# Kernel tuning notes

Measured on AMD Instinct MI355X. Metric: run time of the kernel, lower is better.

## Reference

```python
import jax, jax.numpy as jnp
import numpy as np

N = 50000          # nodes
E = 1_600_000      # edges (avg degree 32)
F = 64             # num_features == hidden dim of every layer
R = 5              # num_rel (edge ratings)
B = 4              # num_base (basis decomposition)
L = 4              # number of RGCN layers (dim=[64,64,64,64])
K = 2048           # nodes with x[:,0]==1 (target user/item nodes)


def setup_inputs() -> dict:
    key = jax.random.key(0)
    ks = jax.random.split(key, 10)
    x = jax.random.normal(ks[0], (N, F), dtype=jnp.float32)
    target_idx = jnp.arange(K, dtype=jnp.int32)
    # mark exactly K target nodes: x[:,0] == 1 iff node index < K
    col0 = (jnp.arange(N) < K).astype(jnp.float32)
    x = x.at[:, 0].set(col0)
    edge_index = jax.random.randint(ks[1], (2, E), 0, N, dtype=jnp.int32)
    edge_type = jax.random.randint(ks[2], (E,), 0, R, dtype=jnp.int32)
    s = 1.0 / np.sqrt(F)
    bases = jax.random.normal(ks[3], (L, B, F, F), dtype=jnp.float32) * s
    comps = jax.random.normal(ks[4], (L, R, B), dtype=jnp.float32) * (1.0 / np.sqrt(B))
    roots = jax.random.normal(ks[5], (L, F, F), dtype=jnp.float32) * s
    biases = jnp.zeros((L, F), dtype=jnp.float32)
    w1 = jax.random.normal(ks[6], (2 * L * F, 128), dtype=jnp.float32) * (1.0 / np.sqrt(2 * L * F))
    b1 = jnp.zeros((128,), dtype=jnp.float32)
    w2 = jax.random.normal(ks[7], (128, 1), dtype=jnp.float32) * (1.0 / np.sqrt(128))
    b2 = jnp.zeros((1,), dtype=jnp.float32)
    return {"x": x, "edge_index": edge_index, "edge_type": edge_type,
            "target_idx": target_idx, "bases": bases, "comps": comps,
            "roots": roots, "biases": biases, "w1": w1, "b1": b1,
            "w2": w2, "b2": b2}


def _rgcn_layer(x, src, dst, etype, bases_l, comp_l, root_l, bias_l):
    # basis decomposition: W_r = sum_b comp[r,b] * bases[b]   -> [R, in, out]
    W = jnp.einsum('rb,bio->rio', comp_l, bases_l)
    # transform every node under every relation, then gather per edge
    H = jnp.einsum('ni,rio->rno', x, W)          # [R, N, out]
    m = H[etype, src]                            # [E, out] per-edge messages
    # per-(target node, relation) MEAN aggregation (PyG RGCNConv semantics)
    seg = dst * R + etype                        # [E]
    sums = jax.ops.segment_sum(m, seg, num_segments=N * R)
    cnts = jax.ops.segment_sum(jnp.ones((m.shape[0],), dtype=x.dtype), seg,
                               num_segments=N * R)
    mean = sums / jnp.maximum(cnts, 1.0)[:, None]
    agg = mean.reshape(N, R, -1).sum(axis=1)     # sum over relations
    return agg + x @ root_l + bias_l


def reference(x, edge_index, edge_type, target_idx, bases, comps, roots,
              biases, w1, b1, w2, b2):
    # inference mode: edge dropout / feature dropout are identity
    src, dst = edge_index[0], edge_index[1]
    h = x
    h_i = []
    for l in range(L):
        h = jnp.tanh(_rgcn_layer(h, src, dst, edge_type,
                                 bases[l], comps[l], roots[l], biases[l]))
        h_i.append(h)
    h_cat = jnp.concatenate(h_i, axis=1)         # [N, sum(dim)] = [N, 256]
    # u and i masks are identical in the source (x[:,0]==1); target_idx holds
    # exactly those node indices, so index gather == boolean mask selection.
    sel = h_cat[target_idx]                      # [K, 256]
    feat = jnp.concatenate([sel, sel], axis=1)   # [K, 512]
    hid = jax.nn.relu(feat @ w1 + b1)
    out = hid @ w2 + b2
    return out[:, 0]
```

## Files before the change

### kernel.cpp

```cpp
#include <hip/hip_runtime.h>
#include <hip/hip_bf16.h>

#define Nn 50000
#define Ee 1600000
#define Ff 64
#define Rr 5
#define Bb 4
#define Ll 4
#define Kk 2048
#define NBK 196
#define SEGB 1280
#define MsegP (NBK*SEGB)
#define NTC ((Nn+63)/64)
#define NCH ((Ee+8191)/8192)
#define WTSL (12*4*64*8)

typedef __attribute__((ext_vector_type(8))) short short8;
typedef __attribute__((ext_vector_type(4))) float v4f;

static __device__ __forceinline__ unsigned short f2b(float f){
  unsigned u = __float_as_uint(f);
  unsigned r = (u + 0x7fffu + ((u>>16)&1u)) >> 16;
  return (unsigned short)r;
}
static __device__ __forceinline__ unsigned packbf(float lo, float hi){
  return (unsigned)f2b(lo) | ((unsigned)f2b(hi) << 16);
}
static __device__ __forceinline__ float2 unpackbf(unsigned u){
  return make_float2(__uint_as_float(u << 16), __uint_as_float(u & 0xffff0000u));
}

#define XB_B 6250
#define IV_B (XB_B+196)
#define WE_B (IV_B+128)
#define WS_B (WE_B+48)
#define TF_B (WS_B+4)
#define MS_B (TF_B+1)
__global__ __launch_bounds__(256) void k_setupA(const float* __restrict__ x, unsigned* __restrict__ xb,
    int* __restrict__ inv, const float* __restrict__ w1, float* __restrict__ w1e,
    const float* __restrict__ bases, const float* __restrict__ comps, const float* __restrict__ roots,
    unsigned short* __restrict__ WTs, int* __restrict__ tflag, int* __restrict__ bcnt,
    unsigned* __restrict__ hA, unsigned* __restrict__ hB)
{
  int b = blockIdx.x, t = threadIdx.x;
  if (b < XB_B){
    int idx = b*256 + t;
    int n = idx >> 5, j = idx & 31;
    float2 v = *(const float2*)&x[(size_t)n*64 + 2*j];
    xb[idx] = packbf(v.x, v.y);
  } else if (b < IV_B){
    int i = (b-XB_B)*256 + t;
    if (i < Nn) inv[i] = -1;
  } else if (b < WE_B){
    int idx = (b-IV_B)*256 + t;
    int i = idx >> 7, j = idx & 127;
    w1e[idx] = w1[i*128 + j] + w1[(i+256)*128 + j];
  } else if (b < WS_B){
    int gid = (b-WE_B)*256 + t;
    int lane = gid & 63, nb = (gid>>6)&3, idx2 = gid>>8;
    int l = idx2/12, kk = idx2 - l*12;
    int o = nb*16 + (lane & 15);
    int kbase = kk*32 + (lane>>4)*8;
    const float* basesl = bases + (size_t)l*Bb*Ff*Ff;
    const float* compsl = comps + (size_t)l*Rr*Bb;
    const float* rootsl = roots + (size_t)l*Ff*Ff;
    unsigned short* wp = WTs + (size_t)gid*8;
    #pragma unroll
    for (int j=0;j<8;j++){
      int k = kbase + j;
      float s;
      if (k < 320){
        int c = k >> 6, i = k & 63;
        s = 0.f;
        #pragma unroll
        for (int bb2=0;bb2<Bb;bb2++)
          s += compsl[c*Bb+bb2] * basesl[(bb2*Ff + i)*Ff + o];
      } else {
        s = rootsl[(k-320)*Ff + o];
      }
      wp[j] = f2b(s);
    }
  } else if (b < TF_B){
    int i = (b-WS_B)*256 + t;
    if (i < NTC) tflag[i] = 0;
  } else {
    if (t < NBK+1) bcnt[t] = 0;
    if (t < 32){
      xb[(size_t)Nn*32 + t] = 0;
      hA[(size_t)Nn*32 + t] = 0;
      hB[(size_t)Nn*32 + t] = 0;
    }
  }
}

__global__ __launch_bounds__(256) void k_setupB(const int* __restrict__ tidx, int* __restrict__ inv,
                                                int* __restrict__ tflag){
  int k = blockIdx.x*256+threadIdx.x;
  if (k < Kk){
    int n = tidx[k];
    inv[n] = k;
    tflag[n >> 6] = 1;
  }
}

__global__ __launch_bounds__(256) void k_bcnt(const int* __restrict__ ei, int* __restrict__ bcnt){
  __shared__ int h[NBK];
  int t = threadIdx.x;
  for (int i=t;i<NBK;i+=256) h[i]=0;
  __syncthreads();
  int base = blockIdx.x*8192;
  for (int i=0;i<32;i++){
    int e = base + i*256 + t;
    if (e < Ee) atomicAdd(&h[ei[Ee+e]>>8], 1);
  }
  __syncthreads();
  for (int i=t;i<NBK;i+=256) if (h[i]) atomicAdd(&bcnt[i], h[i]);
}

__global__ __launch_bounds__(256) void k_bscan(const int* __restrict__ bcnt, int* __restrict__ bbase,
                                               int* __restrict__ bfill, int* __restrict__ rowptr){
  __shared__ int s[256];
  int t = threadIdx.x;
  int v = (t < NBK) ? bcnt[t] : 0;
  s[t] = v; __syncthreads();
  #pragma unroll
  for (int off=1; off<256; off<<=1){
    int x = (t>=off) ? s[t-off] : 0;
    __syncthreads();
    s[t] += x;
    __syncthreads();
  }
  if (t < NBK){ int ex = s[t]-v; bbase[t]=ex; bfill[t]=ex; }
  if (t == 0){ bbase[NBK] = Ee; rowptr[MsegP] = Ee; }
}

__global__ __launch_bounds__(256) void k_bin(const int* __restrict__ ei, const int* __restrict__ et,
                                             int* __restrict__ bfill, unsigned* __restrict__ ebin){
  __shared__ unsigned led[8192];
  __shared__ int h[NBK], gb[NBK];
  int t = threadIdx.x;
  for (int i=t;i<NBK;i+=256) h[i]=0;
  __syncthreads();
  int base = blockIdx.x*8192;
  for (int i=0;i<32;i++){
    int e = base + i*256 + t;
    if (e < Ee){
      int src = ei[e];
      int dst = ei[Ee+e];
      int r = et[e];
      led[i*256+t] = (unsigned)src | ((unsigned)(dst&255)<<16) | ((unsigned)r<<24);
      atomicAdd(&h[dst>>8], 1);
    }
  }
  __syncthreads();
  for (int i=t;i<NBK;i+=256) if (h[i]){ gb[i] = atomicAdd(&bfill[i], h[i]); h[i] = 0; }
  __syncthreads();
  for (int i=0;i<32;i++){
    int e = base + i*256 + t;
    if (e < Ee){
      int b = ei[Ee+e]>>8;
      int off = atomicAdd(&h[b], 1);
      ebin[gb[b]+off] = led[i*256+t];
    }
  }
}

__global__ __launch_bounds__(512) void k_sort(const unsigned* __restrict__ ebin, const int* __restrict__ bbase,
                                              unsigned short* __restrict__ srcs, int* __restrict__ rowptr){
  __shared__ int cntA[SEGB], excA[SEGB];
  int b = blockIdx.x, t = threadIdx.x;
  int base = bbase[b], cnt = bbase[b+1]-base;
  for (int i=t;i<SEGB;i+=512) cntA[i]=0;
  __syncthreads();
  for (int i=t;i<cnt;i+=512){
    unsigned u = ebin[base+i];
    int segl = (int)((u>>24)&7u)*256 + (int)((u>>16)&255u);
    atomicAdd(&cntA[segl], 1);
  }
  __syncthreads();
  for (int i=t;i<SEGB;i+=512) excA[i]=cntA[i];
  __syncthreads();
  for (int off=1; off<SEGB; off<<=1){
    int i0=t, i1=t+512, i2=t+1024;
    int v0 = (i0>=off)? excA[i0-off] : 0;
    int v1 = (i1>=off)? excA[i1-off] : 0;
    int v2 = (i2<SEGB && i2>=off)? excA[i2-off] : 0;
    __syncthreads();
    excA[i0]+=v0;
    excA[i1]+=v1;
    if (i2<SEGB) excA[i2]+=v2;
    __syncthreads();
  }
  for (int i=t;i<SEGB;i+=512){
    int ex = excA[i]-cntA[i];
    excA[i] = ex;
    rowptr[b*SEGB+i] = base + ex;
    cntA[i] = 0;
  }
  __syncthreads();
  for (int i=t;i<cnt;i+=512){
    unsigned u = ebin[base+i];
    int segl = (int)((u>>24)&7u)*256 + (int)((u>>16)&255u);
    int off = atomicAdd(&cntA[segl], 1);
    srcs[base + excA[segl] + off] = (unsigned short)(u & 0xffffu);
  }
}

static __device__ __forceinline__ void gpass(int mys, float* A, int p, int half5, int sub, int li,
                                             const unsigned* __restrict__ h2)
{
  int s0 = __shfl(mys, half5 + p +      sub, 64);
  int s1 = __shfl(mys, half5 + p +  4 + sub, 64);
  int s2 = __shfl(mys, half5 + p +  8 + sub, 64);
  int s3 = __shfl(mys, half5 + p + 12 + sub, 64);
  uint4 g0 = *(const uint4*)&h2[(size_t)s0*32 + li*4];
  uint4 g1 = *(const uint4*)&h2[(size_t)s1*32 + li*4];
  uint4 g2 = *(const uint4*)&h2[(size_t)s2*32 + li*4];
  uint4 g3 = *(const uint4*)&h2[(size_t)s3*32 + li*4];
  float2 f;
  f=unpackbf(g0.x); A[0]+=f.x; A[1]+=f.y;  f=unpackbf(g0.y); A[2]+=f.x; A[3]+=f.y;
  f=unpackbf(g0.z); A[4]+=f.x; A[5]+=f.y;  f=unpackbf(g0.w); A[6]+=f.x; A[7]+=f.y;
  f=unpackbf(g1.x); A[0]+=f.x; A[1]+=f.y;  f=unpackbf(g1.y); A[2]+=f.x; A[3]+=f.y;
  f=unpackbf(g1.z); A[4]+=f.x; A[5]+=f.y;  f=unpackbf(g1.w); A[6]+=f.x; A[7]+=f.y;
  f=unpackbf(g2.x); A[0]+=f.x; A[1]+=f.y;  f=unpackbf(g2.y); A[2]+=f.x; A[3]+=f.y;
  f=unpackbf(g2.z); A[4]+=f.x; A[5]+=f.y;  f=unpackbf(g2.w); A[6]+=f.x; A[7]+=f.y;
  f=unpackbf(g3.x); A[0]+=f.x; A[1]+=f.y;  f=unpackbf(g3.y); A[2]+=f.x; A[3]+=f.y;
  f=unpackbf(g3.z); A[4]+=f.x; A[5]+=f.y;  f=unpackbf(g3.w); A[6]+=f.x; A[7]+=f.y;
}

static __device__ __forceinline__ void tail_gather(float* A, int s, int e, int li,
    const unsigned short* __restrict__ srcs, const unsigned* __restrict__ h2)
{
  for (int i = s; i < e; i++){
    uint4 g = *(const uint4*)&h2[(size_t)srcs[i]*32 + li*4];
    float2 f;
    f=unpackbf(g.x); A[0]+=f.x; A[1]+=f.y;  f=unpackbf(g.y); A[2]+=f.x; A[3]+=f.y;
    f=unpackbf(g.z); A[4]+=f.x; A[5]+=f.y;  f=unpackbf(g.w); A[6]+=f.x; A[7]+=f.y;
  }
}

__global__ __launch_bounds__(256) void k_seg(const unsigned short* __restrict__ srcs,
    const int* __restrict__ rowptr, const unsigned* __restrict__ h2, unsigned* __restrict__ y2)
{
  int tid = threadIdx.x;
  int hw = tid >> 5;
  int l2 = tid & 31, li = l2 & 7, sub = l2 >> 3;
  int half5 = tid & 32;
  int wl = tid & 63;
  int sA = blockIdx.x*16 + hw*2;
  int b = sA / SEGB;
  int segl = sA - b*SEGB;
  int r = segl >> 8;
  int dstA = b*256 + (segl & 255);
  int2 pp = *(const int2*)&rowptr[sA];
  int p2 = rowptr[sA+2];
  int degA = pp.y - pp.x, degB = p2 - pp.y;
  unsigned ldA = srcs[pp.x + l2];
  unsigned ldB = srcs[pp.y + l2];
  int mysA = (l2 < degA) ? (int)ldA : Nn;
  int mysB = (l2 < degB) ? (int)ldB : Nn;
  float aA[8] = {0.f,0.f,0.f,0.f,0.f,0.f,0.f,0.f};
  float aB[8] = {0.f,0.f,0.f,0.f,0.f,0.f,0.f,0.f};

  gpass(mysA, aA, 0, half5, sub, li, h2);
  gpass(mysB, aB, 0, half5, sub, li, h2);
  if (degA > 16) gpass(mysA, aA, 16, half5, sub, li, h2);
  if (degB > 16) gpass(mysB, aB, 16, half5, sub, li, h2);

  if (sub == 0){
    if (degA > 32) tail_gather(aA, pp.x+32, pp.y, li, srcs, h2);
    if (degB > 32) tail_gather(aB, pp.y+32, p2,   li, srcs, h2);
  }
  #pragma unroll
  for (int k=0;k<8;k++){
    aA[k] += __shfl(aA[k], wl^8, 64);
    aB[k] += __shfl(aB[k], wl^8, 64);
  }
  #pragma unroll
  for (int k=0;k<8;k++){
    aA[k] += __shfl(aA[k], wl^16, 64);
    aB[k] += __shfl(aB[k], wl^16, 64);
  }
  if (sub == 0){
    if (dstA < Nn){
      float sc = (degA > 0) ? 1.0f/(float)degA : 0.f;
      uint4 o;
      o.x = packbf(aA[0]*sc, aA[1]*sc);
      o.y = packbf(aA[2]*sc, aA[3]*sc);
      o.z = packbf(aA[4]*sc, aA[5]*sc);
      o.w = packbf(aA[6]*sc, aA[7]*sc);
      *(uint4*)&y2[((size_t)r*Nn + dstA)*32 + li*4] = o;
    }
    if (dstA + 1 < Nn){
      float sc = (degB > 0) ? 1.0f/(float)degB : 0.f;
      uint4 o;
      o.x = packbf(aB[0]*sc, aB[1]*sc);
      o.y = packbf(aB[2]*sc, aB[3]*sc);
      o.z = packbf(aB[4]*sc, aB[5]*sc);
      o.w = packbf(aB[6]*sc, aB[7]*sc);
      *(uint4*)&y2[((size_t)r*Nn + dstA + 1)*32 + li*4] = o;
    }
  }
}

__global__ __launch_bounds__(256) void k_seg_t(const unsigned short* __restrict__ srcs,
    const int* __restrict__ rowptr, const unsigned* __restrict__ h2, unsigned* __restrict__ y2,
    const int* __restrict__ tidx)
{
  int idx = blockIdx.x*8 + (threadIdx.x >> 5);
  if (idx >= Rr*Kk) return;
  int r = idx >> 11;
  int k = idx & (Kk-1);
  int dst = tidx[k];
  int s2 = (dst>>8)*SEGB + r*256 + (dst&255);
  int tid = threadIdx.x;
  int l2 = tid & 31, li = l2 & 7, sub = l2 >> 3;
  int half5 = tid & 32;
  int wl = tid & 63;
  int s = rowptr[s2], e = rowptr[s2+1];
  int deg = e - s;
  unsigned ld = srcs[s + l2];
  int mys = (l2 < deg) ? (int)ld : Nn;
  float a[8] = {0.f,0.f,0.f,0.f,0.f,0.f,0.f,0.f};
  gpass(mys, a, 0, half5, sub, li, h2);
  if (deg > 16) gpass(mys, a, 16, half5, sub, li, h2);
  if (deg > 32 && sub == 0) tail_gather(a, s+32, e, li, srcs, h2);
  #pragma unroll
  for (int q=0;q<8;q++) a[q] += __shfl(a[q], wl^8, 64);
  #pragma unroll
  for (int q=0;q<8;q++) a[q] += __shfl(a[q], wl^16, 64);
  if (sub == 0){
    float sc = (deg > 0) ? 1.0f/(float)deg : 0.f;
    uint4 o;
    o.x = packbf(a[0]*sc, a[1]*sc);
    o.y = packbf(a[2]*sc, a[3]*sc);
    o.z = packbf(a[4]*sc, a[5]*sc);
    o.w = packbf(a[6]*sc, a[7]*sc);
    *(uint4*)&y2[((size_t)r*Nn + dst)*32 + li*4] = o;
  }
}

__global__ __launch_bounds__(256) void k_combm(const unsigned* __restrict__ y2, const unsigned* __restrict__ h2,
    const unsigned short* __restrict__ WTsl, const float* __restrict__ bias,
    unsigned short* __restrict__ hn, const int* __restrict__ inv, float* __restrict__ sel,
    int layer, const int* __restrict__ tflag)
{
  if (layer == Ll-1 && tflag[blockIdx.x] == 0) return;
  int wv = threadIdx.x >> 6, lane = threadIdx.x & 63;
  int m = lane & 15, q = lane >> 4;
  int row = blockIdx.x*64 + wv*16 + m;
  int rowc = (row < Nn) ? row : Nn-1;
  const char* y2c = (const char*)y2;
  const char* h2c = (const char*)h2;
  const unsigned short* wl = WTsl + (size_t)lane*8;

  v4f acc0 = {0.f,0.f,0.f,0.f}, acc1 = {0.f,0.f,0.f,0.f},
      acc2 = {0.f,0.f,0.f,0.f}, acc3 = {0.f,0.f,0.f,0.f};

  #pragma unroll
  for (int kk=0; kk<12; kk++){
    const char* base = (kk < 10)
      ? y2c + ((size_t)((kk>>1)*Nn + rowc))*128 + (size_t)(kk&1)*64
      : h2c + ((size_t)rowc)*128 + (size_t)(kk&1)*64;
    short8 a = *(const short8*)(base + q*16);
    const unsigned short* wb = wl + kk*2048;
    short8 b0 = *(const short8*)(wb);
    short8 b1 = *(const short8*)(wb + 512);
    short8 b2 = *(const short8*)(wb + 1024);
    short8 b3 = *(const short8*)(wb + 1536);
    acc0 = __builtin_amdgcn_mfma_f32_16x16x32_bf16(a, b0, acc0, 0, 0, 0);
    acc1 = __builtin_amdgcn_mfma_f32_16x16x32_bf16(a, b1, acc1, 0, 0, 0);
    acc2 = __builtin_amdgcn_mfma_f32_16x16x32_bf16(a, b2, acc2, 0, 0, 0);
    acc3 = __builtin_amdgcn_mfma_f32_16x16x32_bf16(a, b3, acc3, 0, 0, 0);
  }

  float bc0 = bias[ 0 + m], bc1 = bias[16 + m], bc2 = bias[32 + m], bc3 = bias[48 + m];
  #pragma unroll
  for (int j=0;j<4;j++){
    int node = blockIdx.x*64 + wv*16 + q*4 + j;
    if (node < Nn){
      float r0 = tanhf(acc0[j] + bc0);
      float r1 = tanhf(acc1[j] + bc1);
      float r2 = tanhf(acc2[j] + bc2);
      float r3 = tanhf(acc3[j] + bc3);
      if (layer != Ll-1){
        unsigned short* hp = &hn[(size_t)node*64];
        hp[ 0 + m] = f2b(r0);
        hp[16 + m] = f2b(r1);
        hp[32 + m] = f2b(r2);
        hp[48 + m] = f2b(r3);
      }
      int k = inv[node];
      if (k >= 0){
        float* sp = &sel[(size_t)k*256 + layer*64];
        sp[ 0 + m] = r0;
        sp[16 + m] = r1;
        sp[32 + m] = r2;
        sp[48 + m] = r3;
      }
    }
  }
}

__global__ __launch_bounds__(128) void k_mlp(const float* __restrict__ sel, const float* __restrict__ w1e,
    const float* __restrict__ b1, const float* __restrict__ w2, const float* __restrict__ b2,
    float* __restrict__ out)
{
  __shared__ float sfeat[256];
  __shared__ float partial[2];
  int k = blockIdx.x, j = threadIdx.x;
  for (int idx=j; idx<256; idx+=128) sfeat[idx] = sel[(size_t)k*256 + idx];
  __syncthreads();
  float a = b1[j];
  for (int i=0;i<256;i++) a += sfeat[i] * w1e[i*128 + j];
  a = fmaxf(a, 0.f);
  float v = a * w2[j];
  #pragma unroll
  for (int off=32; off>0; off>>=1) v += __shfl_down(v, off, 64);
  if ((j & 63) == 0) partial[j>>6] = v;
  __syncthreads();
  if (j == 0) out[k] = partial[0] + partial[1] + b2[0];
}

extern "C" void kernel_launch(void* const* d_in, const int* in_sizes, int n_in,
                              void* d_out, int out_size, void* d_ws, size_t ws_size,
                              hipStream_t stream){
  const float* x     = (const float*)d_in[0];
  const int*  ei     = (const int*)d_in[1];
  const int*  et     = (const int*)d_in[2];
  const int*  tidx   = (const int*)d_in[3];
  const float* bases = (const float*)d_in[4];
  const float* comps = (const float*)d_in[5];
  const float* roots = (const float*)d_in[6];
  const float* biases= (const float*)d_in[7];
  const float* w1    = (const float*)d_in[8];
  const float* b1    = (const float*)d_in[9];
  const float* w2    = (const float*)d_in[10];
  const float* b2    = (const float*)d_in[11];
  float* out = (float*)d_out;

  char* wsp = (char*)d_ws;
  size_t off = 0;
  auto alloc = [&](size_t bytes)->void*{ void* p = wsp + off; off += (bytes + 255) & ~size_t(255); return p; };
  unsigned* xb    = (unsigned*)alloc(sizeof(unsigned)*((size_t)Nn+1)*32);
  unsigned* hA    = (unsigned*)alloc(sizeof(unsigned)*((size_t)Nn+1)*32);
  unsigned* hB    = (unsigned*)alloc(sizeof(unsigned)*((size_t)Nn+1)*32);
  unsigned* y2    = (unsigned*)alloc(sizeof(unsigned)*(size_t)Rr*Nn*32);
  unsigned* ebin  = (unsigned*)alloc(sizeof(unsigned)*(size_t)Ee);
  int*      bcnt  = (int*)  alloc(sizeof(int)*(NBK+1));
  int*      bbase = (int*)  alloc(sizeof(int)*(NBK+1));
  int*      bfill = (int*)  alloc(sizeof(int)*(NBK));
  int*      rowptr= (int*)  alloc(sizeof(int)*(MsegP+1));
  unsigned short* srcs = (unsigned short*)alloc(sizeof(unsigned short)*((size_t)Ee+64));
  unsigned short* WTs  = (unsigned short*)alloc(sizeof(unsigned short)*(size_t)Ll*WTSL);
  float*    sel   = (float*)alloc(sizeof(float)*(size_t)Kk*256);
  float*    w1e   = (float*)alloc(sizeof(float)*256*128);
  int*      inv   = (int*)  alloc(sizeof(int)*(size_t)Nn);
  int*      tflag = (int*)  alloc(sizeof(int)*NTC);
  (void)ws_size;

  k_setupA<<<MS_B+1, 256, 0, stream>>>(x, xb, inv, w1, w1e, bases, comps, roots,
                                       WTs, tflag, bcnt, hA, hB);
  k_setupB<<<(Kk+255)/256, 256, 0, stream>>>(tidx, inv, tflag);
  k_bcnt<<<NCH, 256, 0, stream>>>(ei, bcnt);
  k_bscan<<<1, 256, 0, stream>>>(bcnt, bbase, bfill, rowptr);
  k_bin<<<NCH, 256, 0, stream>>>(ei, et, bfill, ebin);
  k_sort<<<NBK, 512, 0, stream>>>(ebin, bbase, srcs, rowptr);

  const unsigned* hc = xb;
  unsigned* hn = hA;
  for (int l=0;l<Ll;l++){
    if (l < Ll-1)
      k_seg<<<MsegP/16, 256, 0, stream>>>(srcs, rowptr, hc, y2);
    else
      k_seg_t<<<(Rr*Kk+7)/8, 256, 0, stream>>>(srcs, rowptr, hc, y2, tidx);
    k_combm<<<NTC, 256, 0, stream>>>(y2, hc, WTs + (size_t)l*WTSL, biases + (size_t)l*Ff,
                                     (unsigned short*)hn, inv, sel, l, tflag);
    hc = hn;
    hn = (hn == hA) ? hB : hA;
  }
  k_mlp<<<Kk, 128, 0, stream>>>(sel, w1e, b1, w2, b2, out);
}
```

Baseline: 333.7 us.

## Fuse segment aggregation and MFMA combine into one per-16-node kernel

Merges the per-relation mean aggregation (k_seg/k_seg_t) with the MFMA-based combine (k_combm) into a single kernel. Each block handles 16 destination nodes across all 5 relations, staging the aggregated bf16 means in a swizzled shared-memory tile instead of writing and re-reading the global y2 buffer. This removes a global round trip for 5*N*64 bf16 values and one launch per layer. In exchange, each block loops serially over relations, which reduces gather parallelism per block. The last-layer target skip now uses 16-node granularity flags, so the last layer gathers for whole 16-node blocks rather than only the target nodes.

```diff
diff --git a/kernel.cpp b/kernel.cpp
--- a/kernel.cpp
+++ b/kernel.cpp
@@ -11,7 +11,7 @@
 #define NBK 196
 #define SEGB 1280
 #define MsegP (NBK*SEGB)
-#define NTC ((Nn+63)/64)
+#define NT16 3125
 #define NCH ((Ee+8191)/8192)
 #define WTSL (12*4*64*8)
 
@@ -34,12 +34,12 @@
 #define IV_B (XB_B+196)
 #define WE_B (IV_B+128)
 #define WS_B (WE_B+48)
-#define TF_B (WS_B+4)
+#define TF_B (WS_B+13)
 #define MS_B (TF_B+1)
 __global__ __launch_bounds__(256) void k_setupA(const float* __restrict__ x, unsigned* __restrict__ xb,
     int* __restrict__ inv, const float* __restrict__ w1, float* __restrict__ w1e,
     const float* __restrict__ bases, const float* __restrict__ comps, const float* __restrict__ roots,
-    unsigned short* __restrict__ WTs, int* __restrict__ tflag, int* __restrict__ bcnt,
+    unsigned short* __restrict__ WTs, int* __restrict__ t16f, int* __restrict__ bcnt,
     unsigned* __restrict__ hA, unsigned* __restrict__ hB)
 {
   int b = blockIdx.x, t = threadIdx.x;
@@ -82,7 +82,7 @@
     }
   } else if (b < TF_B){
     int i = (b-WS_B)*256 + t;
-    if (i < NTC) tflag[i] = 0;
+    if (i < NT16) t16f[i] = 0;
   } else {
     if (t < NBK+1) bcnt[t] = 0;
     if (t < 32){
@@ -94,12 +94,12 @@
 }
 
 __global__ __launch_bounds__(256) void k_setupB(const int* __restrict__ tidx, int* __restrict__ inv,
-                                                int* __restrict__ tflag){
+                                                int* __restrict__ t16f){
   int k = blockIdx.x*256+threadIdx.x;
   if (k < Kk){
     int n = tidx[k];
     inv[n] = k;
-    tflag[n >> 6] = 1;
+    t16f[n >> 4] = 1;
   }
 }
 
@@ -239,166 +239,103 @@
   }
 }
 
-__global__ __launch_bounds__(256) void k_seg(const unsigned short* __restrict__ srcs,
-    const int* __restrict__ rowptr, const unsigned* __restrict__ h2, unsigned* __restrict__ y2)
+__global__ __launch_bounds__(256, 4) void k_fused(const unsigned short* __restrict__ srcs,
+    const int* __restrict__ rowptr, const unsigned* __restrict__ h2,
+    const unsigned short* __restrict__ WTsl, const float* __restrict__ bias,
+    unsigned short* __restrict__ hn, const int* __restrict__ inv, float* __restrict__ sel,
+    int layer, const int* __restrict__ t16f)
 {
+  if (layer == Ll-1 && t16f[blockIdx.x] == 0) return;
+  __shared__ __align__(16) unsigned short ytile[5*16*64];
+  char* yb = (char*)ytile;
   int tid = threadIdx.x;
   int hw = tid >> 5;
   int l2 = tid & 31, li = l2 & 7, sub = l2 >> 3;
   int half5 = tid & 32;
   int wl = tid & 63;
-  int sA = blockIdx.x*16 + hw*2;
-  int b = sA / SEGB;
-  int segl = sA - b*SEGB;
-  int r = segl >> 8;
-  int dstA = b*256 + (segl & 255);
-  int2 pp = *(const int2*)&rowptr[sA];
-  int p2 = rowptr[sA+2];
-  int degA = pp.y - pp.x, degB = p2 - pp.y;
-  unsigned ldA = srcs[pp.x + l2];
-  unsigned ldB = srcs[pp.y + l2];
-  int mysA = (l2 < degA) ? (int)ldA : Nn;
-  int mysB = (l2 < degB) ? (int)ldB : Nn;
-  float aA[8] = {0.f,0.f,0.f,0.f,0.f,0.f,0.f,0.f};
-  float aB[8] = {0.f,0.f,0.f,0.f,0.f,0.f,0.f,0.f};
-
-  gpass(mysA, aA, 0, half5, sub, li, h2);
-  gpass(mysB, aB, 0, half5, sub, li, h2);
-  if (degA > 16) gpass(mysA, aA, 16, half5, sub, li, h2);
-  if (degB > 16) gpass(mysB, aB, 16, half5, sub, li, h2);
-
-  if (sub == 0){
-    if (degA > 32) tail_gather(aA, pp.x+32, pp.y, li, srcs, h2);
-    if (degB > 32) tail_gather(aB, pp.y+32, p2,   li, srcs, h2);
-  }
-  #pragma unroll
-  for (int k=0;k<8;k++){
-    aA[k] += __shfl(aA[k], wl^8, 64);
-    aB[k] += __shfl(aB[k], wl^8, 64);
-  }
-  #pragma unroll
-  for (int k=0;k<8;k++){
-    aA[k] += __shfl(aA[k], wl^16, 64);
-    aB[k] += __shfl(aB[k], wl^16, 64);
-  }
-  if (sub == 0){
-    if (dstA < Nn){
-      float sc = (degA > 0) ? 1.0f/(float)degA : 0.f;
-      uint4 o;
-      o.x = packbf(aA[0]*sc, aA[1]*sc);
-      o.y = packbf(aA[2]*sc, aA[3]*sc);
-      o.z = packbf(aA[4]*sc, aA[5]*sc);
-      o.w = packbf(aA[6]*sc, aA[7]*sc);
-      *(uint4*)&y2[((size_t)r*Nn + dstA)*32 + li*4] = o;
-    }
-    if (dstA + 1 < Nn){
-      float sc = (degB > 0) ? 1.0f/(float)degB : 0.f;
-      uint4 o;
-      o.x = packbf(aB[0]*sc, aB[1]*sc);
-      o.y = packbf(aB[2]*sc, aB[3]*sc);
-      o.z = packbf(aB[4]*sc, aB[5]*sc);
-      o.w = packbf(aB[6]*sc, aB[7]*sc);
-      *(uint4*)&y2[((size_t)r*Nn + dstA + 1)*32 + li*4] = o;
-    }
-  }
-}
-
-__global__ __launch_bounds__(256) void k_seg_t(const unsigned short* __restrict__ srcs,
-    const int* __restrict__ rowptr, const unsigned* __restrict__ h2, unsigned* __restrict__ y2,
-    const int* __restrict__ tidx)
-{
-  int idx = blockIdx.x*8 + (threadIdx.x >> 5);
-  if (idx >= Rr*Kk) return;
-  int r = idx >> 11;
-  int k = idx & (Kk-1);
-  int dst = tidx[k];
-  int s2 = (dst>>8)*SEGB + r*256 + (dst&255);
-  int tid = threadIdx.x;
-  int l2 = tid & 31, li = l2 & 7, sub = l2 >> 3;
-  int half5 = tid & 32;
-  int wl = tid & 63;
-  int s = rowptr[s2], e = rowptr[s2+1];
-  int deg = e - s;
-  unsigned ld = srcs[s + l2];
-  int mys = (l2 < deg) ? (int)ld : Nn;
-  float a[8] = {0.f,0.f,0.f,0.f,0.f,0.f,0.f,0.f};
-  gpass(mys, a, 0, half5, sub, li, h2);
-  if (deg > 16) gpass(mys, a, 16, half5, sub, li, h2);
-  if (deg > 32 && sub == 0) tail_gather(a, s+32, e, li, srcs, h2);
-  #pragma unroll
-  for (int q=0;q<8;q++) a[q] += __shfl(a[q], wl^8, 64);
-  #pragma unroll
-  for (int q=0;q<8;q++) a[q] += __shfl(a[q], wl^16, 64);
-  if (sub == 0){
-    float sc = (deg > 0) ? 1.0f/(float)deg : 0.f;
-    uint4 o;
-    o.x = packbf(a[0]*sc, a[1]*sc);
-    o.y = packbf(a[2]*sc, a[3]*sc);
-    o.z = packbf(a[4]*sc, a[5]*sc);
-    o.w = packbf(a[6]*sc, a[7]*sc);
-    *(uint4*)&y2[((size_t)r*Nn + dst)*32 + li*4] = o;
-  }
-}
-
-__global__ __launch_bounds__(256) void k_combm(const unsigned* __restrict__ y2, const unsigned* __restrict__ h2,
-    const unsigned short* __restrict__ WTsl, const float* __restrict__ bias,
-    unsigned short* __restrict__ hn, const int* __restrict__ inv, float* __restrict__ sel,
-    int layer, const int* __restrict__ tflag)
-{
-  if (layer == Ll-1 && tflag[blockIdx.x] == 0) return;
-  int wv = threadIdx.x >> 6, lane = threadIdx.x & 63;
+  int d0 = blockIdx.x * 16;
+  int sbase = (d0 >> 8)*SEGB + (d0 & 255) + hw*2;
+  int rl0 = hw*2;
+
+  #pragma unroll 1
+  for (int r = 0; r < Rr; ++r){
+    int sA = sbase + r*256;
+    int2 pp = *(const int2*)&rowptr[sA];
+    int p2 = rowptr[sA+2];
+    int degA = pp.y - pp.x, degB = p2 - pp.y;
+    unsigned ldA = srcs[pp.x + l2];
+    unsigned ldB = srcs[pp.y + l2];
+    int mysA = (l2 < degA) ? (int)ldA : Nn;
+    int mysB = (l2 < degB) ? (int)ldB : Nn;
+    float aA[8] = {0.f,0.f,0.f,0.f,0.f,0.f,0.f,0.f};
+    float aB[8] = {0.f,0.f,0.f,0.f,0.f,0.f,0.f,0.f};
+
+    gpass(mysA, aA, 0, half5, sub, li, h2);
+    gpass(mysB, aB, 0, half5, sub, li, h2);
+    if (degA > 16) gpass(mysA, aA, 16, half5, sub, li, h2);
+    if (degB > 16) gpass(mysB, aB, 16, half5, sub, li, h2);
+    if (sub == 0){
+      if (degA > 32) tail_gather(aA, pp.x+32, pp.y, li, srcs, h2);
+      if (degB > 32) tail_gather(aB, pp.y+32, p2,   li, srcs, h2);
+    }
+    #pragma unroll
+    for (int k=0;k<8;k++){
+      aA[k] += __shfl(aA[k], wl^8, 64);
+      aB[k] += __shfl(aB[k], wl^8, 64);
+    }
+    #pragma unroll
+    for (int k=0;k<8;k++){
+      aA[k] += __shfl(aA[k], wl^16, 64);
+      aB[k] += __shfl(aB[k], wl^16, 64);
+    }
+    if (sub == 0){
+      float scA = (degA > 0) ? 1.0f/(float)degA : 0.f;
+      float scB = (degB > 0) ? 1.0f/(float)degB : 0.f;
+      uint4 oA, oB;
+      oA.x = packbf(aA[0]*scA, aA[1]*scA);
+      oA.y = packbf(aA[2]*scA, aA[3]*scA);
+      oA.z = packbf(aA[4]*scA, aA[5]*scA);
+      oA.w = packbf(aA[6]*scA, aA[7]*scA);
+      oB.x = packbf(aB[0]*scB, aB[1]*scB);
+      oB.y = packbf(aB[2]*scB, aB[3]*scB);
+      oB.z = packbf(aB[4]*scB, aB[5]*scB);
+      oB.w = packbf(aB[6]*scB, aB[7]*scB);
+      int trA = r*16 + rl0;
+      *(uint4*)(yb + (( trA   *128 + li*16) ^ (( rl0   &7)<<4))) = oA;
+      *(uint4*)(yb + (((trA+1)*128 + li*16) ^ (((rl0+1)&7)<<4))) = oB;
+    }
+  }
+  __syncthreads();
+
+  int wv = tid >> 6;
+  int lane = tid & 63;
   int m = lane & 15, q = lane >> 4;
-  int row = blockIdx.x*64 + wv*16 + m;
-  int rowc = (row < Nn) ? row : Nn-1;
-  const char* y2c = (const char*)y2;
+  const unsigned short* wp = WTsl + (size_t)lane*8 + (size_t)wv*512;
   const char* h2c = (const char*)h2;
-  const unsigned short* wl = WTsl + (size_t)lane*8;
-
-  v4f acc0 = {0.f,0.f,0.f,0.f}, acc1 = {0.f,0.f,0.f,0.f},
-      acc2 = {0.f,0.f,0.f,0.f}, acc3 = {0.f,0.f,0.f,0.f};
-
+  int rowm = d0 + m;
+  v4f acc = {0.f,0.f,0.f,0.f};
   #pragma unroll
   for (int kk=0; kk<12; kk++){
-    const char* base = (kk < 10)
-      ? y2c + ((size_t)((kk>>1)*Nn + rowc))*128 + (size_t)(kk&1)*64
-      : h2c + ((size_t)rowc)*128 + (size_t)(kk&1)*64;
-    short8 a = *(const short8*)(base + q*16);
-    const unsigned short* wb = wl + kk*2048;
-    short8 b0 = *(const short8*)(wb);
-    short8 b1 = *(const short8*)(wb + 512);
-    short8 b2 = *(const short8*)(wb + 1024);
-    short8 b3 = *(const short8*)(wb + 1536);
-    acc0 = __builtin_amdgcn_mfma_f32_16x16x32_bf16(a, b0, acc0, 0, 0, 0);
-    acc1 = __builtin_amdgcn_mfma_f32_16x16x32_bf16(a, b1, acc1, 0, 0, 0);
-    acc2 = __builtin_amdgcn_mfma_f32_16x16x32_bf16(a, b2, acc2, 0, 0, 0);
-    acc3 = __builtin_amdgcn_mfma_f32_16x16x32_bf16(a, b3, acc3, 0, 0, 0);
-  }
-
-  float bc0 = bias[ 0 + m], bc1 = bias[16 + m], bc2 = bias[32 + m], bc3 = bias[48 + m];
+    short8 a;
+    if (kk < 10){
+      int tr = (kk>>1)*16 + m;
+      a = *(const short8*)(yb + ((tr*128 + (kk&1)*64 + q*16) ^ ((m&7)<<4)));
+    } else {
+      a = *(const short8*)(h2c + (size_t)rowm*128 + (size_t)(kk&1)*64 + q*16);
+    }
+    short8 bf = *(const short8*)(wp + (size_t)kk*2048);
+    acc = __builtin_amdgcn_mfma_f32_16x16x32_bf16(a, bf, acc, 0, 0, 0);
+  }
+  float bc = bias[wv*16 + m];
   #pragma unroll
   for (int j=0;j<4;j++){
-    int node = blockIdx.x*64 + wv*16 + q*4 + j;
-    if (node < Nn){
-      float r0 = tanhf(acc0[j] + bc0);
-      float r1 = tanhf(acc1[j] + bc1);
-      float r2 = tanhf(acc2[j] + bc2);
-      float r3 = tanhf(acc3[j] + bc3);
-      if (layer != Ll-1){
-        unsigned short* hp = &hn[(size_t)node*64];
-        hp[ 0 + m] = f2b(r0);
-        hp[16 + m] = f2b(r1);
-        hp[32 + m] = f2b(r2);
-        hp[48 + m] = f2b(r3);
-      }
-      int k = inv[node];
-      if (k >= 0){
-        float* sp = &sel[(size_t)k*256 + layer*64];
-        sp[ 0 + m] = r0;
-        sp[16 + m] = r1;
-        sp[32 + m] = r2;
-        sp[48 + m] = r3;
-      }
-    }
+    int node = d0 + q*4 + j;
+    float rres = tanhf(acc[j] + bc);
+    if (layer != Ll-1)
+      hn[(size_t)node*64 + wv*16 + m] = f2b(rres);
+    int k = inv[node];
+    if (k >= 0)
+      sel[(size_t)k*256 + layer*64 + wv*16 + m] = rres;
   }
 }
 
@@ -445,7 +382,6 @@
   unsigned* xb    = (unsigned*)alloc(sizeof(unsigned)*((size_t)Nn+1)*32);
   unsigned* hA    = (unsigned*)alloc(sizeof(unsigned)*((size_t)Nn+1)*32);
   unsigned* hB    = (unsigned*)alloc(sizeof(unsigned)*((size_t)Nn+1)*32);
-  unsigned* y2    = (unsigned*)alloc(sizeof(unsigned)*(size_t)Rr*Nn*32);
   unsigned* ebin  = (unsigned*)alloc(sizeof(unsigned)*(size_t)Ee);
   int*      bcnt  = (int*)  alloc(sizeof(int)*(NBK+1));
   int*      bbase = (int*)  alloc(sizeof(int)*(NBK+1));
@@ -456,12 +392,12 @@
   float*    sel   = (float*)alloc(sizeof(float)*(size_t)Kk*256);
   float*    w1e   = (float*)alloc(sizeof(float)*256*128);
   int*      inv   = (int*)  alloc(sizeof(int)*(size_t)Nn);
-  int*      tflag = (int*)  alloc(sizeof(int)*NTC);
+  int*      t16f  = (int*)  alloc(sizeof(int)*NT16);
   (void)ws_size;
 
   k_setupA<<<MS_B+1, 256, 0, stream>>>(x, xb, inv, w1, w1e, bases, comps, roots,
-                                       WTs, tflag, bcnt, hA, hB);
-  k_setupB<<<(Kk+255)/256, 256, 0, stream>>>(tidx, inv, tflag);
+                                       WTs, t16f, bcnt, hA, hB);
+  k_setupB<<<(Kk+255)/256, 256, 0, stream>>>(tidx, inv, t16f);
   k_bcnt<<<NCH, 256, 0, stream>>>(ei, bcnt);
   k_bscan<<<1, 256, 0, stream>>>(bcnt, bbase, bfill, rowptr);
   k_bin<<<NCH, 256, 0, stream>>>(ei, et, bfill, ebin);
@@ -470,12 +406,9 @@
   const unsigned* hc = xb;
   unsigned* hn = hA;
   for (int l=0;l<Ll;l++){
-    if (l < Ll-1)
-      k_seg<<<MsegP/16, 256, 0, stream>>>(srcs, rowptr, hc, y2);
-    else
-      k_seg_t<<<(Rr*Kk+7)/8, 256, 0, stream>>>(srcs, rowptr, hc, y2, tidx);
-    k_combm<<<NTC, 256, 0, stream>>>(y2, hc, WTs + (size_t)l*WTSL, biases + (size_t)l*Ff,
-                                     (unsigned short*)hn, inv, sel, l, tflag);
+    k_fused<<<NT16, 256, 0, stream>>>(srcs, rowptr, hc, WTs + (size_t)l*WTSL,
+                                      biases + (size_t)l*Ff, (unsigned short*)hn,
+                                      inv, sel, l, t16f);
     hc = hn;
     hn = (hn == hA) ? hB : hA;
   }
```

Result: faster. 322.2 us (-3.5%).
